# Kernel tuning notes

Hardware: AMD Instinct MI355X
Metric: run time of the kernel (lower is better)

Reference implementation:

```python
import jax, jax.numpy as jnp
import numpy as np

B, L, D = 2, 2048, 512
H = 8
DH = D // H
MAX_DIST = 2048
DFC = 2048


def setup_inputs() -> dict:
    key = jax.random.key(0)
    ks = jax.random.split(key, 12)
    w = lambda k, shape: (jax.random.normal(k, shape, jnp.float32) * 0.02)
    x = jax.random.normal(ks[0], (B, L, D), jnp.float32)
    # additive causal mask: 0 on/below diagonal, -1e9 above
    mask = jnp.where(jnp.triu(jnp.ones((L, L), bool), 1), -1e9, 0.0).astype(jnp.float32)
    return {
        "x": x,
        "mask": mask,
        "wq": w(ks[1], (D, D)), "bq": jnp.zeros((D,), jnp.float32),
        "wk": w(ks[2], (D, D)), "bk": jnp.zeros((D,), jnp.float32),
        "wv": w(ks[3], (D, D)), "bv": jnp.zeros((D,), jnp.float32),
        "rel_emb": w(ks[4], (MAX_DIST, D)),
        "w1": w(ks[5], (D, DFC)), "b1": jnp.zeros((DFC,), jnp.float32),
        "w2": w(ks[6], (DFC, D)), "b2": jnp.zeros((D,), jnp.float32),
    }


def skew(q_e):
    # Huang et al. sec 3.4: pad one column on the left, reshape (L, L+1)->(L+1, L), drop first row
    b, h, l, _ = q_e.shape
    padded = jnp.pad(q_e, ((0, 0), (0, 0), (0, 0), (1, 0)))  # (B,H,L,L+1)
    return padded.reshape(b, h, l + 1, l)[:, :, 1:, :]        # (B,H,L,L)


def reference(x, mask, wq, bq, wk, bk, wv, bv, rel_emb, w1, b1, w2, b2):
    b, l, d = x.shape
    q = (x @ wq + bq).reshape(b, l, H, DH)
    k = (x @ wk + bk).reshape(b, l, H, DH)
    v = (x @ wv + bv).reshape(b, l, H, DH)
    # relative position embeddings for the last l positions
    e = rel_emb[rel_emb.shape[0] - l:].reshape(l, H, DH)       # (L,H,DH)
    q_e = jnp.einsum('blhd,mhd->bhlm', q, e)                   # QE^T
    s_rel = skew(q_e)
    qk = jnp.einsum('blhd,bmhd->bhlm', q, k)                   # QK^T
    logits = (qk + s_rel) / jnp.sqrt(jnp.float32(DH)) + mask
    a = jax.nn.softmax(logits, axis=-1)
    attn = jnp.einsum('bhlm,bmhd->blhd', a, v).reshape(b, l, d)
    h = jax.nn.relu(attn @ w1 + b1)  # dropout is identity in eval mode
    return h @ w2 + b2
```

## Files before the change

### kernel.cpp

```cpp
#include <hip/hip_runtime.h>
#include <cstdint>

#define B_   2
#define L_   2048
#define D_   512
#define H_   8
#define DH_  64
#define DFC_ 2048

typedef unsigned short ushort_t;
typedef __attribute__((ext_vector_type(8))) short bf16x8;
typedef __attribute__((ext_vector_type(4))) short bf16x4;
typedef __attribute__((ext_vector_type(4))) float f32x4;

#define MFMA32(A, Bv, C) __builtin_amdgcn_mfma_f32_16x16x32_bf16(A, Bv, C, 0, 0, 0)
#define MFMA16(A, Bv, C) __builtin_amdgcn_mfma_f32_16x16x16bf16_1k(A, Bv, C, 0, 0, 0)

__device__ __forceinline__ ushort_t f32_bf16(float f) {
  unsigned u = __float_as_uint(f);
  u += 0x7FFFu + ((u >> 16) & 1u);
  return (ushort_t)(u >> 16);
}
__device__ __forceinline__ float bf16_f32(ushort_t u) {
  return __uint_as_float(((unsigned)u) << 16);
}

__device__ __forceinline__ void gl_lds16(const ushort_t* g, ushort_t* l) {
  __builtin_amdgcn_global_load_lds(
      (const __attribute__((address_space(1))) void*)(const void*)g,
      (__attribute__((address_space(3))) void*)l, 16, 0, 0);
}

__global__ __launch_bounds__(256)
void pack_all(const float* __restrict__ x, const float* __restrict__ rel,
              const float* __restrict__ wq, const float* __restrict__ wk,
              const float* __restrict__ wv, const float* __restrict__ w1,
              const float* __restrict__ w2,
              ushort_t* __restrict__ xb, ushort_t* __restrict__ relb,
              ushort_t* __restrict__ wqkvT, ushort_t* __restrict__ w1T,
              ushort_t* __restrict__ w2T) {
  __shared__ float T[64 * 65];
  const int bid = blockIdx.x;
  const int t = threadIdx.x;
  if (bid < 1536) {
    const float* in = (bid < 1024) ? x : rel;
    ushort_t* out = (bid < 1024) ? xb : relb;
    const int base = (bid < 1024) ? bid : (bid - 1024);
    int i = (base * 256 + t) * 8;
    float4 a = *(const float4*)(in + i);
    float4 b = *(const float4*)(in + i + 4);
    union { bf16x8 v; ushort_t s[8]; } u;
    u.s[0] = f32_bf16(a.x); u.s[1] = f32_bf16(a.y);
    u.s[2] = f32_bf16(a.z); u.s[3] = f32_bf16(a.w);
    u.s[4] = f32_bf16(b.x); u.s[5] = f32_bf16(b.y);
    u.s[6] = f32_bf16(b.z); u.s[7] = f32_bf16(b.w);
    *(bf16x8*)(out + i) = u.v;
    return;
  }
  const int id = bid - 1536;
  const float* in; ushort_t* out; int K, N, bx, by;
  if (id < 192) {
    int z = id >> 6, r = id & 63;
    in = (z == 0) ? wq : (z == 1) ? wk : wv;
    out = wqkvT + (size_t)z * 512 * 512;
    K = 512; N = 512; bx = r & 7; by = r >> 3;
  } else if (id < 448) {
    int r = id - 192;
    in = w1; out = w1T; K = 512; N = 2048; bx = r & 31; by = r >> 5;
  } else {
    int r = id - 448;
    in = w2; out = w2T; K = 2048; N = 512; bx = r & 7; by = r >> 3;
  }
  const int n0 = bx * 64, k0 = by * 64;
  {
    const int kr = t >> 2, c0 = (t & 3) * 16;
    const float* src = in + (size_t)(k0 + kr) * N + n0 + c0;
#pragma unroll
    for (int u = 0; u < 4; ++u) {
      float4 f = *(const float4*)(src + u * 4);
      T[kr * 65 + c0 + u * 4 + 0] = f.x;
      T[kr * 65 + c0 + u * 4 + 1] = f.y;
      T[kr * 65 + c0 + u * 4 + 2] = f.z;
      T[kr * 65 + c0 + u * 4 + 3] = f.w;
    }
  }
  __syncthreads();
  const int nr = t >> 2, kc0 = (t & 3) * 16;
  union { bf16x8 v; ushort_t s[8]; } o0, o1;
#pragma unroll
  for (int j = 0; j < 8; ++j) {
    o0.s[j] = f32_bf16(T[(kc0 + j) * 65 + nr]);
    o1.s[j] = f32_bf16(T[(kc0 + 8 + j) * 65 + nr]);
  }
  ushort_t* dst = out + (size_t)(n0 + nr) * K + k0 + kc0;
  *(bf16x8*)dst = o0.v;
  *(bf16x8*)(dst + 8) = o1.v;
}

template <int MODE>
__global__ __launch_bounds__(256, 4)
void gemm_mfma(const ushort_t* __restrict__ A, const ushort_t* __restrict__ Bt,
               const float* __restrict__ b0p, const float* __restrict__ b1p,
               const float* __restrict__ b2p,
               void* __restrict__ out0, void* __restrict__ out1, void* __restrict__ out2,
               int M, int N, int K, int ksplit) {
  __shared__ ushort_t As[2][64 * 32];
  __shared__ ushort_t Bs[2][128 * 32];

  const int t  = threadIdx.x;
  const int wv = t >> 6, ln = t & 63;
  const int l16 = ln & 15, lg = ln >> 4;
  const int n0 = blockIdx.x * 128, m0 = blockIdx.y * 64;
  const int mw = (wv >> 1) * 32, nw = (wv & 1) * 64;

  const int kchunk = K / ksplit;
  const int kbeg = blockIdx.z * kchunk, kend = kbeg + kchunk;

  f32x4 acc[2][4] = {};

  auto stage = [&](int k0, int b) {
    {
      const int s = wv * 64 + ln;
      const int row = s >> 2, cs = s & 3;
      const int g = cs ^ ((row >> 1) & 3);
      gl_lds16(A + (size_t)(m0 + row) * K + k0 + g * 8, &As[b][wv * 512]);
    }
#pragma unroll
    for (int i = 0; i < 2; ++i) {
      const int s = (i * 4 + wv) * 64 + ln;
      const int row = s >> 2, cs = s & 3;
      const int g = cs ^ ((row >> 1) & 3);
      gl_lds16(Bt + (size_t)(n0 + row) * K + k0 + g * 8, &Bs[b][(i * 4 + wv) * 512]);
    }
  };

  stage(kbeg, 0);
  int buf = 0;
  for (int k0 = kbeg; k0 < kend; k0 += 32) {
    __syncthreads();
    if (k0 + 32 < kend) stage(k0 + 32, buf ^ 1);

    bf16x8 af[2], bfr[4];
#pragma unroll
    for (int mi = 0; mi < 2; ++mi) {
      const int ri = mw + mi * 16 + l16;
      af[mi] = *(const bf16x8*)&As[buf][ri * 32 + ((lg ^ ((ri >> 1) & 3)) * 8)];
    }
#pragma unroll
    for (int ni = 0; ni < 4; ++ni) {
      const int rj = nw + ni * 16 + l16;
      bfr[ni] = *(const bf16x8*)&Bs[buf][rj * 32 + ((lg ^ ((rj >> 1) & 3)) * 8)];
    }
#pragma unroll
    for (int mi = 0; mi < 2; ++mi)
#pragma unroll
      for (int ni = 0; ni < 4; ++ni)
        acc[mi][ni] = MFMA32(af[mi], bfr[ni], acc[mi][ni]);
    buf ^= 1;
  }

  if (MODE == 0) {
    float* outp = (blockIdx.z == 0) ? (float*)out0 : (float*)out1;
#pragma unroll
    for (int mi = 0; mi < 2; ++mi)
#pragma unroll
      for (int reg = 0; reg < 4; ++reg) {
        const int m = m0 + mw + mi * 16 + lg * 4 + reg;
#pragma unroll
        for (int ni = 0; ni < 4; ++ni) {
          const int c = n0 + nw + ni * 16 + l16;
          outp[(size_t)m * N + c] = acc[mi][ni][reg];
        }
      }
  } else if (MODE == 1) {
    ushort_t* outp = (ushort_t*)out0;
#pragma unroll
    for (int mi = 0; mi < 2; ++mi)
#pragma unroll
      for (int reg = 0; reg < 4; ++reg) {
        const int m = m0 + mw + mi * 16 + lg * 4 + reg;
#pragma unroll
        for (int ni = 0; ni < 4; ++ni) {
          const int c = n0 + nw + ni * 16 + l16;
          float v = acc[mi][ni][reg] + b0p[c];
          outp[(size_t)m * N + c] = f32_bf16(fmaxf(v, 0.f));
        }
      }
  } else {
#pragma unroll
    for (int mi = 0; mi < 2; ++mi)
#pragma unroll
      for (int reg = 0; reg < 4; ++reg) {
        const int m = m0 + mw + mi * 16 + lg * 4 + reg;
        const int b = m >> 11, l = m & (L_ - 1);
#pragma unroll
        for (int ni = 0; ni < 4; ++ni) {
          const int c = n0 + nw + ni * 16 + l16;
          const int which = c >> 9, cc = c & 511;
          const int h = cc >> 6, dh = cc & 63;
          const float* bias = (which == 0) ? b0p : (which == 1) ? b1p : b2p;
          float v = acc[mi][ni][reg] + bias[cc];
          if (which == 0) {
            ((ushort_t*)out0)[(((size_t)b * H_ + h) * L_ + l) * DH_ + dh] =
                f32_bf16(v * 0.125f);
          } else if (which == 1) {
            ((ushort_t*)out1)[(((size_t)b * H_ + h) * L_ + l) * DH_ + dh] = f32_bf16(v);
          } else {
            ((ushort_t*)out2)[(((size_t)b * H_ + h) * DH_ + dh) * L_ + l] = f32_bf16(v);
          }
        }
      }
  }
}

__global__ __launch_bounds__(256)
void ffn2_add(float* __restrict__ out, const float* __restrict__ p1,
              const float* __restrict__ bias) {
  int i = (blockIdx.x * 256 + threadIdx.x) * 4;
  float4 a = *(const float4*)(out + i);
  float4 b = *(const float4*)(p1 + i);
  float4 bb = *(const float4*)(bias + (i & (D_ - 1)));
  a.x += b.x + bb.x; a.y += b.y + bb.y;
  a.z += b.z + bb.z; a.w += b.w + bb.w;
  *(float4*)(out + i) = a;
}

__global__ __launch_bounds__(256, 3)
void attn_mfma(const ushort_t* __restrict__ q16, const ushort_t* __restrict__ k16,
               const ushort_t* __restrict__ vT, const ushort_t* __restrict__ relb,
               ushort_t* __restrict__ Opart, float* __restrict__ Lpart) {
  __shared__ ushort_t Ks[2][64 * 64];
  __shared__ ushort_t Vs[2][64 * 64];
  __shared__ ushort_t Rc[64 * 136];

  const int t   = threadIdx.x;
  const int wv  = t >> 6;
  const int ln  = t & 63;
  const int l16 = ln & 15;
  const int lg  = ln >> 4;
  const int bh  = blockIdx.x;
  const int yy  = blockIdx.y;
  const int qb  = 31 - ((yy < 16) ? yy : (47 - yy));
  const int z   = blockIdx.z;
  const int i0  = qb * 64;
  const int mid = (qb + 2) >> 1;
  const int kbeg = z ? mid : 0;
  const int kend = z ? (qb + 1) : mid;

  const ushort_t* qh = q16 + (size_t)bh * L_ * DH_;
  const ushort_t* kh = k16 + (size_t)bh * L_ * DH_;
  const ushort_t* vh = vT + (size_t)bh * DH_ * L_;
  const ushort_t* relh = relb + (bh & 7) * DH_;

  const int r64i = wv * 16 + l16;
  const int rrow = r64i * 136;

  bf16x8 qf0, qf1;
  {
    const ushort_t* qr = qh + (size_t)(i0 + r64i) * DH_ + lg * 8;
    qf0 = *(const bf16x8*)(qr);
    qf1 = *(const bf16x8*)(qr + 32);
  }

  const f32x4 zf = {0.f, 0.f, 0.f, 0.f};
  f32x4 Of[4] = {zf, zf, zf, zf};
  float lsum = 0.f;
  bf16x8 eA[4], eB[4];

  auto stageKV = [&](int j0, int b) {
#pragma unroll
    for (int i = 0; i < 2; ++i) {
      const int s = (i * 4 + wv) * 64 + ln;
      const int row = s >> 3, c = s & 7;
      const int g = c ^ (row & 7);
      gl_lds16(kh + (size_t)(j0 + row) * DH_ + g * 8, &Ks[b][(i * 4 + wv) * 512]);
      gl_lds16(vh + (size_t)row * L_ + j0 + g * 8, &Vs[b][(i * 4 + wv) * 512]);
    }
  };

  auto load_E = [&](int mbase) {
#pragma unroll
    for (int cb = 0; cb < 4; ++cb) {
      const ushort_t* e = relh + (size_t)(mbase + cb * 16 + l16) * D_ + lg * 8;
      eA[cb] = *(const bf16x8*)(e);
      eB[cb] = *(const bf16x8*)(e + 32);
    }
  };

  auto mfma_R = [&](int slotbase) {
#pragma unroll
    for (int cb = 0; cb < 4; ++cb) {
      f32x4 r = MFMA32(eA[cb], qf0, zf);
      r = MFMA32(eB[cb], qf1, r);
      ushort4 w;
      w.x = f32_bf16(r[0]); w.y = f32_bf16(r[1]);
      w.z = f32_bf16(r[2]); w.w = f32_bf16(r[3]);
      *(ushort4*)&Rc[rrow + slotbase + cb * 16 + lg * 4] = w;
      if (slotbase == 0 && cb == 0 && lg == 0)
        *(ushort4*)&Rc[rrow + 128] = w;
    }
  };

  if (kbeg < kend) {
    load_E(L_ - 64 - i0 + kbeg * 64);
    stageKV(kbeg * 64, kbeg & 1);
    mfma_R((kbeg & 1) * 64);
    if (kbeg < qb) load_E(L_ - 64 - i0 + (kbeg + 1) * 64);

    for (int kb = kbeg; kb < kend; ++kb) {
      const int j0 = kb * 64;
      const int buf = kb & 1;
      __syncthreads();
      if (kb + 1 < kend) stageKV(j0 + 64, buf ^ 1);
      if (kb < qb) mfma_R(((kb + 1) & 1) * 64);
      if (kb + 1 < qb) load_E(L_ - 64 - i0 + (kb + 2) * 64);

      f32x4 sf[4];
#pragma unroll
      for (int cb = 0; cb < 4; ++cb) {
        const int j = cb * 16 + l16;
        const int sw = j & 7;
        bf16x8 k0 = *(const bf16x8*)&Ks[buf][j * 64 + ((lg ^ sw) * 8)];
        bf16x8 k1 = *(const bf16x8*)&Ks[buf][j * 64 + (((lg + 4) ^ sw) * 8)];
        f32x4 s = MFMA32(k0, qf0, zf);
        sf[cb] = MFMA32(k1, qf1, s);
      }

      const bool diag = (kb == qb);
      bf16x4 pa[4];
#pragma unroll
      for (int cb = 0; cb < 4; ++cb) {
        const int jj0 = cb * 16 + lg * 4;
        const int base = (j0 + jj0 + 63 - r64i) & 127;
        union { bf16x4 v; ushort_t s[4]; } pk;
#pragma unroll
        for (int reg = 0; reg < 4; ++reg) {
          float x = sf[cb][reg] + bf16_f32(Rc[rrow + base + reg]);
          if (diag && (jj0 + reg) > r64i) x = -1e30f;
          float p = __expf(x);
          lsum += p;
          pk.s[reg] = f32_bf16(p);
        }
        pa[cb] = pk.v;
      }

#pragma unroll
      for (int cb2 = 0; cb2 < 4; ++cb2) {
        const int dh = cb2 * 16 + l16;
        const int sw = dh & 7;
        const ushort_t* vrow = &Vs[buf][dh * 64];
#pragma unroll
        for (int cb = 0; cb < 4; ++cb) {
          const int cc = cb * 2 + (lg >> 1);
          bf16x4 vf = *(const bf16x4*)&vrow[((cc ^ sw) * 8) + (lg & 1) * 4];
          Of[cb2] = MFMA16(vf, pa[cb], Of[cb2]);
        }
      }
    }
  }

  float tot = lsum;
  tot += __shfl_xor(tot, 16);
  tot += __shfl_xor(tot, 32);
  if (lg == 0)
    Lpart[((size_t)(z * 16 + bh)) * L_ + i0 + r64i] = tot;
  ushort_t* orow = Opart + (((size_t)(z * 16 + bh)) * L_ + i0 + r64i) * DH_;
#pragma unroll
  for (int cb2 = 0; cb2 < 4; ++cb2) {
    ushort4 w;
    w.x = f32_bf16(Of[cb2][0]); w.y = f32_bf16(Of[cb2][1]);
    w.z = f32_bf16(Of[cb2][2]); w.w = f32_bf16(Of[cb2][3]);
    *(ushort4*)&orow[cb2 * 16 + lg * 4] = w;
  }
}

__global__ __launch_bounds__(256)
void attn_combine(const ushort_t* __restrict__ Opart, const float* __restrict__ Lpart,
                  ushort_t* __restrict__ attnb) {
  const int g = blockIdx.x * 256 + threadIdx.x;
  const int dh4 = g & 15, i = (g >> 4) & (L_ - 1), bh = g >> 15;
  const size_t o0 = (((size_t)bh * L_ + i) * DH_) + dh4 * 4;
  const size_t zs = (size_t)16 * L_ * DH_;
  ushort4 a = *(const ushort4*)(Opart + o0);
  ushort4 b = *(const ushort4*)(Opart + o0 + zs);
  const float l = Lpart[(size_t)bh * L_ + i] + Lpart[(size_t)(16 + bh) * L_ + i];
  const float inv = 1.f / l;
  ushort4 o;
  o.x = f32_bf16((bf16_f32(a.x) + bf16_f32(b.x)) * inv);
  o.y = f32_bf16((bf16_f32(a.y) + bf16_f32(b.y)) * inv);
  o.z = f32_bf16((bf16_f32(a.z) + bf16_f32(b.z)) * inv);
  o.w = f32_bf16((bf16_f32(a.w) + bf16_f32(b.w)) * inv);
  const int bb = bh >> 3, h = bh & 7;
  *(ushort4*)(attnb + ((size_t)(bb * L_ + i)) * D_ + h * DH_ + dh4 * 4) = o;
}

extern "C" void kernel_launch(void* const* d_in, const int* in_sizes, int n_in,
                              void* d_out, int out_size, void* d_ws, size_t ws_size,
                              hipStream_t stream) {
  const float* x   = (const float*)d_in[0];
  const float* wq  = (const float*)d_in[2];
  const float* bq  = (const float*)d_in[3];
  const float* wk  = (const float*)d_in[4];
  const float* bk  = (const float*)d_in[5];
  const float* wv  = (const float*)d_in[6];
  const float* bv  = (const float*)d_in[7];
  const float* rel = (const float*)d_in[8];
  const float* w1  = (const float*)d_in[9];
  const float* b1  = (const float*)d_in[10];
  const float* w2  = (const float*)d_in[11];
  const float* b2  = (const float*)d_in[12];

  char* wsb = (char*)d_ws;
  const size_t MB = 1u << 20;
  ushort_t* xb     = (ushort_t*)(wsb + 0 * MB);
  ushort_t* attnb  = (ushort_t*)(wsb + 0 * MB);
  ushort_t* wqkvT  = (ushort_t*)(wsb + 4 * MB);
  ushort_t* w1T    = (ushort_t*)(wsb + 6 * MB);
  ushort_t* w2T    = (ushort_t*)(wsb + 8 * MB);
  ushort_t* relb   = (ushort_t*)(wsb + 10 * MB);
  ushort_t* q16    = (ushort_t*)(wsb + 12 * MB);
  ushort_t* k16    = (ushort_t*)(wsb + 16 * MB);
  ushort_t* vTb    = (ushort_t*)(wsb + 20 * MB);
  ushort_t* Opart  = (ushort_t*)(wsb + 24 * MB);
  float*    Lpart  = (float*)(wsb + 40 * MB);
  ushort_t* hidb   = (ushort_t*)(wsb + 24 * MB);
  float*    p1     = (float*)(wsb + 12 * MB);
  float*    out    = (float*)d_out;

  dim3 blk(256);
  pack_all<<<dim3(2240), blk, 0, stream>>>(x, rel, wq, wk, wv, w1, w2,
                                           xb, relb, wqkvT, w1T, w2T);
  gemm_mfma<2><<<dim3(12, 64), blk, 0, stream>>>(
      xb, wqkvT, bq, bk, bv, q16, k16, vTb, B_ * L_, 1536, D_, 1);
  attn_mfma<<<dim3(16, 32, 2), blk, 0, stream>>>(q16, k16, vTb, relb, Opart, Lpart);
  attn_combine<<<dim3(2048), blk, 0, stream>>>(Opart, Lpart, attnb);
  gemm_mfma<1><<<dim3(16, 64), blk, 0, stream>>>(
      attnb, w1T, b1, nullptr, nullptr, hidb, nullptr, nullptr,
      B_ * L_, DFC_, D_, 1);
  gemm_mfma<0><<<dim3(4, 64, 2), blk, 0, stream>>>(
      hidb, w2T, nullptr, nullptr, nullptr, out, p1, nullptr,
      B_ * L_, D_, DFC_, 2);
  ffn2_add<<<dim3(2048), blk, 0, stream>>>(out, p1, b2);
}
```

Measured before the change: 220.5 us.

## Load GEMM operands directly from global memory into registers, bypassing LDS

The GEMM kernel drops its double-buffered shared-memory staging and barriers. Each wave now loads its MFMA fragments straight from global memory into registers, prefetching the next k-step into a register double buffer. This removes LDS traffic and __syncthreads, but loses intra-block reuse: waves sharing rows of A or B fetch them separately, and each lane reads only 16 bytes per row per step. That raises L2/global traffic and may leave loads poorly coalesced.

```diff
diff --git a/kernel.cpp b/kernel.cpp
--- a/kernel.cpp
+++ b/kernel.cpp
@@ -99,14 +99,11 @@
 
 template <int MODE>
 __global__ __launch_bounds__(256, 4)
-void gemm_mfma(const ushort_t* __restrict__ A, const ushort_t* __restrict__ Bt,
+void gemm_flat(const ushort_t* __restrict__ A, const ushort_t* __restrict__ Bt,
                const float* __restrict__ b0p, const float* __restrict__ b1p,
                const float* __restrict__ b2p,
                void* __restrict__ out0, void* __restrict__ out1, void* __restrict__ out2,
                int M, int N, int K, int ksplit) {
-  __shared__ ushort_t As[2][64 * 32];
-  __shared__ ushort_t Bs[2][128 * 32];
-
   const int t  = threadIdx.x;
   const int wv = t >> 6, ln = t & 63;
   const int l16 = ln & 15, lg = ln >> 4;
@@ -116,47 +113,41 @@
   const int kchunk = K / ksplit;
   const int kbeg = blockIdx.z * kchunk, kend = kbeg + kchunk;
 
+  const ushort_t* Ar0 = A + (size_t)(m0 + mw + l16) * K;
+  const ushort_t* Ar1 = A + (size_t)(m0 + mw + 16 + l16) * K;
+  const ushort_t* Br0 = Bt + (size_t)(n0 + nw + l16) * K;
+  const ushort_t* Br1 = Bt + (size_t)(n0 + nw + 16 + l16) * K;
+  const ushort_t* Br2 = Bt + (size_t)(n0 + nw + 32 + l16) * K;
+  const ushort_t* Br3 = Bt + (size_t)(n0 + nw + 48 + l16) * K;
+
   f32x4 acc[2][4] = {};
 
-  auto stage = [&](int k0, int b) {
-    {
-      const int s = wv * 64 + ln;
-      const int row = s >> 2, cs = s & 3;
-      const int g = cs ^ ((row >> 1) & 3);
-      gl_lds16(A + (size_t)(m0 + row) * K + k0 + g * 8, &As[b][wv * 512]);
-    }
-#pragma unroll
-    for (int i = 0; i < 2; ++i) {
-      const int s = (i * 4 + wv) * 64 + ln;
-      const int row = s >> 2, cs = s & 3;
-      const int g = cs ^ ((row >> 1) & 3);
-      gl_lds16(Bt + (size_t)(n0 + row) * K + k0 + g * 8, &Bs[b][(i * 4 + wv) * 512]);
-    }
-  };
-
-  stage(kbeg, 0);
-  int buf = 0;
+  bf16x8 a0c, a1c, b0c, b1c, b2c, b3c;
+  bf16x8 a0n, a1n, b0n, b1n, b2n, b3n;
+  {
+    const int ka = kbeg + lg * 8;
+    a0c = *(const bf16x8*)(Ar0 + ka); a1c = *(const bf16x8*)(Ar1 + ka);
+    b0c = *(const bf16x8*)(Br0 + ka); b1c = *(const bf16x8*)(Br1 + ka);
+    b2c = *(const bf16x8*)(Br2 + ka); b3c = *(const bf16x8*)(Br3 + ka);
+  }
+
   for (int k0 = kbeg; k0 < kend; k0 += 32) {
-    __syncthreads();
-    if (k0 + 32 < kend) stage(k0 + 32, buf ^ 1);
-
-    bf16x8 af[2], bfr[4];
-#pragma unroll
-    for (int mi = 0; mi < 2; ++mi) {
-      const int ri = mw + mi * 16 + l16;
-      af[mi] = *(const bf16x8*)&As[buf][ri * 32 + ((lg ^ ((ri >> 1) & 3)) * 8)];
-    }
-#pragma unroll
-    for (int ni = 0; ni < 4; ++ni) {
-      const int rj = nw + ni * 16 + l16;
-      bfr[ni] = *(const bf16x8*)&Bs[buf][rj * 32 + ((lg ^ ((rj >> 1) & 3)) * 8)];
-    }
-#pragma unroll
-    for (int mi = 0; mi < 2; ++mi)
-#pragma unroll
-      for (int ni = 0; ni < 4; ++ni)
-        acc[mi][ni] = MFMA32(af[mi], bfr[ni], acc[mi][ni]);
-    buf ^= 1;
+    if (k0 + 32 < kend) {
+      const int ka = k0 + 32 + lg * 8;
+      a0n = *(const bf16x8*)(Ar0 + ka); a1n = *(const bf16x8*)(Ar1 + ka);
+      b0n = *(const bf16x8*)(Br0 + ka); b1n = *(const bf16x8*)(Br1 + ka);
+      b2n = *(const bf16x8*)(Br2 + ka); b3n = *(const bf16x8*)(Br3 + ka);
+    }
+    acc[0][0] = MFMA32(a0c, b0c, acc[0][0]);
+    acc[0][1] = MFMA32(a0c, b1c, acc[0][1]);
+    acc[0][2] = MFMA32(a0c, b2c, acc[0][2]);
+    acc[0][3] = MFMA32(a0c, b3c, acc[0][3]);
+    acc[1][0] = MFMA32(a1c, b0c, acc[1][0]);
+    acc[1][1] = MFMA32(a1c, b1c, acc[1][1]);
+    acc[1][2] = MFMA32(a1c, b2c, acc[1][2]);
+    acc[1][3] = MFMA32(a1c, b3c, acc[1][3]);
+    a0c = a0n; a1c = a1n;
+    b0c = b0n; b1c = b1n; b2c = b2n; b3c = b3n;
   }
 
   if (MODE == 0) {
@@ -430,14 +421,14 @@
   dim3 blk(256);
   pack_all<<<dim3(2240), blk, 0, stream>>>(x, rel, wq, wk, wv, w1, w2,
                                            xb, relb, wqkvT, w1T, w2T);
-  gemm_mfma<2><<<dim3(12, 64), blk, 0, stream>>>(
+  gemm_flat<2><<<dim3(12, 64), blk, 0, stream>>>(
       xb, wqkvT, bq, bk, bv, q16, k16, vTb, B_ * L_, 1536, D_, 1);
   attn_mfma<<<dim3(16, 32, 2), blk, 0, stream>>>(q16, k16, vTb, relb, Opart, Lpart);
   attn_combine<<<dim3(2048), blk, 0, stream>>>(Opart, Lpart, attnb);
-  gemm_mfma<1><<<dim3(16, 64), blk, 0, stream>>>(
+  gemm_flat<1><<<dim3(16, 64), blk, 0, stream>>>(
       attnb, w1T, b1, nullptr, nullptr, hidb, nullptr, nullptr,
       B_ * L_, DFC_, D_, 1);
-  gemm_mfma<0><<<dim3(4, 64, 2), blk, 0, stream>>>(
+  gemm_flat<0><<<dim3(4, 64, 2), blk, 0, stream>>>(
       hidb, w2T, nullptr, nullptr, nullptr, out, p1, nullptr,
       B_ * L_, D_, DFC_, 2);
   ffn2_add<<<dim3(2048), blk, 0, stream>>>(out, p1, b2);
```

Measured after the change: 295.3 us. +33.9%, slower.
